# Performance work log

Hardware: AMD Instinct MI355X
Metric: run time of the kernel (lower is better)

Reference implementation:

```python
import jax, jax.numpy as jnp
import numpy as np

B, C, N = 2, 256, 8192
H = W = 64
C4 = C // 4
EPS = 1e-5


def bn(x, gamma, beta, mean, var):
    # eval-mode batchnorm over channel axis 1
    shape = (1, -1) + (1,) * (x.ndim - 2)
    inv = gamma * jax.lax.rsqrt(var + EPS)
    return x * inv.reshape(shape) + (beta - mean * inv).reshape(shape)


def conv1x1(x, w, b):
    # w: (Cout, Cin)
    return jnp.einsum('bchw,oc->bohw', x, w) + b.reshape(1, -1, 1, 1)


def conv2d(x, w, b=None, padding='VALID', groups=1, lhs_dilation=None):
    y = jax.lax.conv_general_dilated(
        x, w, window_strides=(1, 1), padding=padding,
        lhs_dilation=lhs_dilation, feature_group_count=groups,
        dimension_numbers=('NCHW', 'OIHW', 'NCHW'))
    return y if b is None else y + b.reshape(1, -1, 1, 1)


def lift_net(x, w1, b1, w2, b2, axis):
    # DAWN predictor/updater: ReflectionPad(2,1) -> conv k=4 along axis (C4->2C4)
    # -> ReLU -> 1x1 conv (2C4->C4) -> Tanh
    pad = [(0, 0)] * 4
    pad[axis] = (2, 1)
    xp = jnp.pad(x, pad, mode='reflect')
    k = w1[:, :, None, :] if axis == 3 else w1[:, :, :, None]
    h = jax.nn.relu(conv2d(xp, k, b1))
    return jnp.tanh(conv1x1(h, w2, b2))


def lifting(x, pw, axis):
    # pw = (w1, b1, w2, b2), each with leading net axis [P, U]
    w1, b1, w2, b2 = pw
    sl_e = [slice(None)] * 4; sl_e[axis] = slice(0, None, 2)
    sl_o = [slice(None)] * 4; sl_o[axis] = slice(1, None, 2)
    x_even, x_odd = x[tuple(sl_e)], x[tuple(sl_o)]
    d = x_odd - lift_net(x_even, w1[0], b1[0], w2[0], b2[0], axis)
    c = x_even + lift_net(d, w1[1], b1[1], w2[1], b2[1], axis)
    return c, d


def wavelet2d(x, w1, b1, w2, b2):
    # leading axes of weights: (scheme[horizontal, vertical], net[P, U])
    c, d = lifting(x, (w1[0], b1[0], w2[0], b2[0]), axis=3)  # split along W
    v = (w1[1], b1[1], w2[1], b2[1])                          # shared vertical weights
    LL, LH = lifting(c, v, axis=2)
    HL, HH = lifting(d, v, axis=2)
    return LL, LH, HL, HH


def convT(x, w, b):
    # torch ConvTranspose2d(k=4, stride=2, pad=1); w: (Cin, Cout, 4, 4)
    wc = jnp.flip(w, (2, 3)).transpose(1, 0, 2, 3)  # (Cout, Cin, 4, 4)
    return conv2d(x, wc, b, padding=[(2, 2), (2, 2)], lhs_dilation=(2, 2))


def _forward(tokens, flatten_mat, bn_gamma, bn_beta, bn_mean, bn_var, red_w, red_b,
             lift_w1, lift_b1, lift_w2, lift_b2,
             ff2_w1, ff2_b1, ff2_w2, ff2_b2, ct2_w, ct2_b,
             bn2_gamma, bn2_beta, bn2_mean, bn2_var,
             ff1_w1, ff1_b1, ff1_w2, ff1_b2, ct1_w, ct1_b,
             bn1_gamma, bn1_beta, bn1_mean, bn1_var,
             dw1_w, dw1_b, dw2_w, dw2_b, scale_w, inflate_idx):
    r = bn(tokens, bn_gamma, bn_beta, bn_mean, bn_var)                       # (B,C,N)
    r = jnp.einsum('bmn,bcn->bcm', flatten_mat, r).reshape(B, C, H, W)       # flatten to grid
    rr = conv1x1(r, red_w, red_b)                                            # (B,C/4,H,W)
    LL1, LH1, HL1, HH1 = wavelet2d(rr, lift_w1[0], lift_b1[0], lift_w2[0], lift_b2[0])
    LL2, LH2, HL2, HH2 = wavelet2d(LL1, lift_w1[1], lift_b1[1], lift_w2[1], lift_b2[1])
    x2 = jnp.concatenate([LL2, LH2, HL2, HH2], 1)                            # (B,C,H/4,W/4)
    y2 = conv1x1(jax.nn.gelu(conv1x1(x2, ff2_w1, ff2_b1), approximate=False), ff2_w2, ff2_b2)
    y2 = bn(convT(y2, ct2_w, ct2_b), bn2_gamma, bn2_beta, bn2_mean, bn2_var) # (B,C/2,H/2,W/2)
    x1 = jnp.concatenate([LL1, LH1, HL1, HH1, y2], 1)                        # (B,1.5C,H/2,W/2)
    y1 = conv1x1(jax.nn.gelu(conv1x1(x1, ff1_w1, ff1_b1), approximate=False), ff1_w2, ff1_b2)
    y1 = bn(convT(y1, ct1_w, ct1_b), bn1_gamma, bn1_beta, bn1_mean, bn1_var) # (B,C,H,W)
    r = r + y1
    r = conv2d(r, dw1_w, dw1_b, padding=[(1, 1), (1, 1)], groups=C)          # depthwise 3x3
    r = conv2d(jax.nn.relu(r), dw2_w, dw2_b, padding=[(1, 1), (1, 1)], groups=C)
    r = r.reshape(B, C, H * W) * scale_w.reshape(1, C, 1)                    # grouped 1x1 conv1d
    r = jnp.take_along_axis(r, inflate_idx, axis=2)                          # inflate gather
    return tokens + r


def setup_inputs() -> dict:
    key = jax.random.key(0)
    ks = iter(jax.random.split(key, 64))
    nrm = lambda shape, s=0.05: jax.random.normal(next(ks), shape, jnp.float32) * s
    uni = lambda shape: jax.random.uniform(next(ks), shape, jnp.float32, 0.5, 1.5)
    return dict(
        tokens=jax.random.normal(next(ks), (B, C, N), jnp.float32),
        flatten_mat=nrm((B, H * W, N), 0.02),
        inflate_idx=jax.random.randint(next(ks), (B, C, N), 0, H * W),
        bn_gamma=jnp.ones((C,), jnp.float32), bn_beta=jnp.zeros((C,), jnp.float32),
        bn_mean=nrm((C,), 0.1), bn_var=uni((C,)),
        red_w=nrm((C4, C)), red_b=nrm((C4,)),
        lift_w1=nrm((2, 2, 2, 2 * C4, C4, 4)), lift_b1=nrm((2, 2, 2, 2 * C4)),
        lift_w2=nrm((2, 2, 2, C4, 2 * C4)), lift_b2=nrm((2, 2, 2, C4)),
        ff2_w1=nrm((C, C)), ff2_b1=nrm((C,)), ff2_w2=nrm((C, C)), ff2_b2=nrm((C,)),
        ct2_w=nrm((C, C // 2, 4, 4)), ct2_b=nrm((C // 2,)),
        bn2_gamma=jnp.ones((C // 2,), jnp.float32), bn2_beta=jnp.zeros((C // 2,), jnp.float32),
        bn2_mean=nrm((C // 2,), 0.1), bn2_var=uni((C // 2,)),
        ff1_w1=nrm((C, C + C // 2)), ff1_b1=nrm((C,)), ff1_w2=nrm((C, C)), ff1_b2=nrm((C,)),
        ct1_w=nrm((C, C, 4, 4)), ct1_b=nrm((C,)),
        bn1_gamma=jnp.ones((C,), jnp.float32), bn1_beta=jnp.zeros((C,), jnp.float32),
        bn1_mean=nrm((C,), 0.1), bn1_var=uni((C,)),
        dw1_w=nrm((C, 1, 3, 3)), dw1_b=nrm((C,)),
        dw2_w=nrm((C, 1, 3, 3)), dw2_b=nrm((C,)),
        scale_w=nrm((C,), 0.2),
    )


def reference(tokens, flatten_mat, inflate_idx, bn_gamma, bn_beta, bn_mean, bn_var,
              red_w, red_b, lift_w1, lift_b1, lift_w2, lift_b2,
              ff2_w1, ff2_b1, ff2_w2, ff2_b2, ct2_w, ct2_b,
              bn2_gamma, bn2_beta, bn2_mean, bn2_var,
              ff1_w1, ff1_b1, ff1_w2, ff1_b2, ct1_w, ct1_b,
              bn1_gamma, bn1_beta, bn1_mean, bn1_var,
              dw1_w, dw1_b, dw2_w, dw2_b, scale_w):
    return _forward(tokens, flatten_mat, bn_gamma, bn_beta, bn_mean, bn_var, red_w, red_b,
                    lift_w1, lift_b1, lift_w2, lift_b2,
                    ff2_w1, ff2_b1, ff2_w2, ff2_b2, ct2_w, ct2_b,
                    bn2_gamma, bn2_beta, bn2_mean, bn2_var,
                    ff1_w1, ff1_b1, ff1_w2, ff1_b2, ct1_w, ct1_b,
                    bn1_gamma, bn1_beta, bn1_mean, bn1_var,
                    dw1_w, dw1_b, dw2_w, dw2_b, scale_w, inflate_idx)
```

## Files before the change

kernel.cpp:

```cpp
#include <hip/hip_runtime.h>
#include <math.h>

#define EPSV 1e-5f

typedef __attribute__((ext_vector_type(8))) short bf16x8;
typedef __attribute__((ext_vector_type(4))) float f32x4;
typedef __attribute__((ext_vector_type(8))) unsigned short u16x8;

__device__ inline unsigned short f2bf(float f) {
    unsigned u = __float_as_uint(f);
    unsigned r = (u + 0x7fffu + ((u >> 16) & 1u)) >> 16;
    return (unsigned short)r;
}

__device__ inline float bf2f(unsigned short h) {
    return __uint_as_float(((unsigned)h) << 16);
}

__device__ inline void gload_lds16(const void* g, void* l) {
    __builtin_amdgcn_global_load_lds(
        (const __attribute__((address_space(1))) void*)g,
        (__attribute__((address_space(3))) void*)l, 16, 0, 0);
}

__global__ __launch_bounds__(256) void bn_to_bf16_kernel(
    const float4* __restrict__ x, ushort4* __restrict__ y,
    const float* __restrict__ g, const float* __restrict__ be,
    const float* __restrict__ mu, const float* __restrict__ va)
{
    int i = blockIdx.x * 256 + threadIdx.x;
    int c = (i >> 11) & 255;
    float s = g[c] * rsqrtf(va[c] + EPSV);
    float t = be[c] - mu[c] * s;
    float4 v = x[i];
    ushort4 h;
    h.x = f2bf(v.x * s + t); h.y = f2bf(v.y * s + t);
    h.z = f2bf(v.z * s + t); h.w = f2bf(v.w * s + t);
    y[i] = h;
}

__global__ __launch_bounds__(256) void flatten_gemm_mfma(
    const unsigned short* __restrict__ A, const float* __restrict__ Bm,
    float* __restrict__ Pbase)
{
    __shared__ __align__(16) unsigned short AS[4][256 * 32];
    __shared__ __align__(16) unsigned short BS[4][64 * 32];
    const int NTT = 64;
    int t = threadIdx.x;
    int wid = t >> 6, lane = t & 63;
    int fid = blockIdx.z * 64 + blockIdx.x;
    int nid = (fid & 7) * 64 + (fid >> 3);
    int n0 = (nid & 63) * 64;
    int zz = nid >> 6;
    int ks = zz & 3, b = zz >> 2;
    const unsigned short* Ab = A + b * (256 * 8192);
    const float* Bb = Bm + (long)b * (4096 * 8192) + (long)n0 * 8192;
    int k0 = ks * 2048;
    int brow = t >> 3, bc8 = t & 7;
    int l15 = lane & 15, kc = lane >> 4;

    f32x4 acc[4][4] = {};

    auto issueA = [&](int tile) {
        int buf = tile & 3;
        int kb = k0 + tile * 32;
        #pragma unroll
        for (int j = 0; j < 4; ++j) {
            int d16 = (wid * 4 + j) * 64 + lane;
            int row = d16 >> 2;
            int ch = (d16 & 3) ^ ((row >> 1) & 3);
            gload_lds16(Ab + row * 8192 + kb + ch * 8, &AS[buf][(wid * 4 + j) * 512]);
        }
    };
    auto loadB = [&](int tile, float4& f0, float4& f1) {
        int kb = k0 + tile * 32;
        f0 = *(const float4*)(Bb + brow * 8192 + kb + bc8 * 4);
        f1 = *(const float4*)(Bb + (brow + 32) * 8192 + kb + bc8 * 4);
    };
    auto writeB = [&](int tile, const float4& f0, const float4& f1) {
        int buf = tile & 3;
        int ch16 = (bc8 >> 1) ^ ((brow >> 1) & 3);
        ushort4 h;
        h.x = f2bf(f0.x); h.y = f2bf(f0.y); h.z = f2bf(f0.z); h.w = f2bf(f0.w);
        *reinterpret_cast<ushort4*>(&BS[buf][brow * 32 + ch16 * 8 + (bc8 & 1) * 4]) = h;
        int rr2 = brow + 32;
        int ch16b = (bc8 >> 1) ^ ((rr2 >> 1) & 3);
        ushort4 h2;
        h2.x = f2bf(f1.x); h2.y = f2bf(f1.y); h2.z = f2bf(f1.z); h2.w = f2bf(f1.w);
        *reinterpret_cast<ushort4*>(&BS[buf][rr2 * 32 + ch16b * 8 + (bc8 & 1) * 4]) = h2;
    };
    auto mmac = [&](int tile) {
        int buf = tile & 3;
        bf16x8 af[4], bfr[4];
        #pragma unroll
        for (int mf = 0; mf < 4; ++mf) {
            int row = wid * 64 + mf * 16 + l15;
            int ch = kc ^ ((row >> 1) & 3);
            af[mf] = *reinterpret_cast<const bf16x8*>(&AS[buf][row * 32 + ch * 8]);
        }
        #pragma unroll
        for (int nf = 0; nf < 4; ++nf) {
            int row = nf * 16 + l15;
            int ch = kc ^ ((row >> 1) & 3);
            bfr[nf] = *reinterpret_cast<const bf16x8*>(&BS[buf][row * 32 + ch * 8]);
        }
        #pragma unroll
        for (int mf = 0; mf < 4; ++mf)
            #pragma unroll
            for (int nf = 0; nf < 4; ++nf)
                acc[mf][nf] = __builtin_amdgcn_mfma_f32_16x16x32_bf16(
                    af[mf], bfr[nf], acc[mf][nf], 0, 0, 0);
    };

    float4 q00, q01, q10, q11, r0, r1;
    loadB(0, q00, q01);
    loadB(1, q10, q11);
    issueA(0);
    issueA(1);

    for (int tau = 0; tau < NTT; ++tau) {
        writeB(tau, q00, q01);
        if (tau == 0)
            asm volatile("s_waitcnt vmcnt(4) lgkmcnt(0)" ::: "memory");
        else if (tau < NTT - 1)
            asm volatile("s_waitcnt vmcnt(6) lgkmcnt(0)" ::: "memory");
        else
            asm volatile("s_waitcnt vmcnt(0) lgkmcnt(0)" ::: "memory");
        __builtin_amdgcn_s_barrier();
        if (tau + 2 < NTT) {
            loadB(tau + 2, r0, r1);
            issueA(tau + 2);
        }
        mmac(tau);
        q00 = q10; q01 = q11; q10 = r0; q11 = r1;
    }

    float* P = Pbase + (long)ks * 2097152;
    float* Cb = P + (b * 256) * 4096 + n0;
    #pragma unroll
    for (int mf = 0; mf < 4; ++mf) {
        int rbase = wid * 64 + mf * 16 + (lane >> 4) * 4;
        #pragma unroll
        for (int nf = 0; nf < 4; ++nf) {
            int col = nf * 16 + (lane & 15);
            #pragma unroll
            for (int r = 0; r < 4; ++r)
                Cb[(rbase + r) * 4096 + col] = acc[mf][nf][r];
        }
    }
}

__global__ __launch_bounds__(256) void add4_t_kernel(
    const float* __restrict__ p, unsigned short* __restrict__ obf)
{
    __shared__ float tl[64][65];
    int t = threadIdx.x;
    int b = blockIdx.z;
    int c0 = blockIdx.y * 64, p0 = blockIdx.x * 64;
    #pragma unroll
    for (int u = 0; u < 16; ++u) {
        int idx = u * 256 + t;
        int cl = idx >> 6, pl = idx & 63;
        long g = (long)(b * 256 + c0 + cl) * 4096 + p0 + pl;
        tl[cl][pl] = p[g] + p[g + 2097152] + p[g + 2 * 2097152] + p[g + 3 * 2097152];
    }
    __syncthreads();
    #pragma unroll
    for (int u = 0; u < 16; ++u) {
        int idx = u * 256 + t;
        int pl = idx >> 6, cl = idx & 63;
        obf[(long)(b * 4096 + p0 + pl) * 256 + c0 + cl] = f2bf(tl[cl][pl]);
    }
}

__global__ __launch_bounds__(256) void wpack_kernel(
    const float* __restrict__ w, unsigned short* __restrict__ wp, int Cout, int Cin)
{
    int id = blockIdx.x * 256 + threadIdx.x;
    int nc8 = Cin >> 3;
    int cch = id % nc8;
    int rest = id / nc8;
    int o = rest % Cout;
    int pt = rest / Cout;
    if (pt >= 16) return;
    int par = pt >> 2, tap = pt & 3;
    int py = par >> 1, px = par & 1, u = tap >> 1, v = tap & 1;
    int tf = (3 - py - 2 * u) * 4 + (3 - px - 2 * v);
    u16x8 h;
    #pragma unroll
    for (int e = 0; e < 8; ++e)
        h[e] = f2bf(w[((cch * 8 + e) * Cout + o) * 16 + tf]);
    *reinterpret_cast<u16x8*>(&wp[((pt * Cout + o) * Cin) + cch * 8]) = h;
}

template<int NF>
__global__ __launch_bounds__(256) void conv1x1_mfma(
    const unsigned short* __restrict__ xbf, const float* __restrict__ w,
    const float* __restrict__ bias, float* __restrict__ of32,
    unsigned short* __restrict__ obf, int Cin, int Cout, int P, int act)
{
    constexpr int BP = NF * 64;
    __shared__ __align__(16) unsigned short XS[2][BP * 32];
    __shared__ __align__(16) unsigned short WS[2][64 * 32];
    int t = threadIdx.x;
    int wid = t >> 6, lane = t & 63;
    int b = blockIdx.z;
    int p0 = blockIdx.x * BP, o0 = blockIdx.y * 64;
    const unsigned short* xb = xbf + (long)b * P * Cin;
    int wm = t >> 2, wq = t & 3;
    int chunks = Cin >> 5;

    f32x4 acc[4][NF] = {};

    #pragma unroll
    for (int j = 0; j < NF; ++j) {
        int d16 = (wid * NF + j) * 64 + lane;
        int p = d16 >> 2;
        int ch = (d16 & 3) ^ ((p >> 1) & 3);
        gload_lds16(xb + (long)(p0 + p) * Cin + ch * 8, &XS[0][(wid * NF + j) * 512]);
    }
    float4 wr0 = *(const float4*)(w + (o0 + wm) * Cin + wq * 8);
    float4 wr1 = *(const float4*)(w + (o0 + wm) * Cin + wq * 8 + 4);
    __syncthreads();

    for (int cc = 0; cc < chunks; ++cc) {
        int cur = cc & 1;
        {
            int chq = wq ^ ((wm >> 1) & 3);
            u16x8 h;
            h[0] = f2bf(wr0.x); h[1] = f2bf(wr0.y); h[2] = f2bf(wr0.z); h[3] = f2bf(wr0.w);
            h[4] = f2bf(wr1.x); h[5] = f2bf(wr1.y); h[6] = f2bf(wr1.z); h[7] = f2bf(wr1.w);
            *reinterpret_cast<u16x8*>(&WS[cur][wm * 32 + chq * 8]) = h;
        }
        __syncthreads();

        if (cc < chunks - 1) {
            int kn = (cc + 1) * 32;
            #pragma unroll
            for (int j = 0; j < NF; ++j) {
                int d16 = (wid * NF + j) * 64 + lane;
                int p = d16 >> 2;
                int ch = (d16 & 3) ^ ((p >> 1) & 3);
                gload_lds16(xb + (long)(p0 + p) * Cin + kn + ch * 8,
                            &XS[cur ^ 1][(wid * NF + j) * 512]);
            }
            wr0 = *(const float4*)(w + (o0 + wm) * Cin + kn + wq * 8);
            wr1 = *(const float4*)(w + (o0 + wm) * Cin + kn + wq * 8 + 4);
        }

        int l15 = lane & 15, kc = lane >> 4;
        bf16x8 af[4], bfr[NF];
        #pragma unroll
        for (int mf = 0; mf < 4; ++mf) {
            int row = mf * 16 + l15;
            int ch = kc ^ ((row >> 1) & 3);
            af[mf] = *reinterpret_cast<const bf16x8*>(&WS[cur][row * 32 + ch * 8]);
        }
        #pragma unroll
        for (int nf = 0; nf < NF; ++nf) {
            int row = wid * (NF * 16) + nf * 16 + l15;
            int ch = kc ^ ((row >> 1) & 3);
            bfr[nf] = *reinterpret_cast<const bf16x8*>(&XS[cur][row * 32 + ch * 8]);
        }
        #pragma unroll
        for (int mf = 0; mf < 4; ++mf)
            #pragma unroll
            for (int nf = 0; nf < NF; ++nf)
                acc[mf][nf] = __builtin_amdgcn_mfma_f32_16x16x32_bf16(
                    af[mf], bfr[nf], acc[mf][nf], 0, 0, 0);
        __syncthreads();
    }

    int l15 = lane & 15, kc4 = lane >> 4;
    #pragma unroll
    for (int mf = 0; mf < 4; ++mf) {
        #pragma unroll
        for (int nf = 0; nf < NF; ++nf) {
            int p = wid * (NF * 16) + nf * 16 + l15;
            ushort4 hb;
            #pragma unroll
            for (int r = 0; r < 4; ++r) {
                int m = mf * 16 + kc4 * 4 + r;
                float v = acc[mf][nf][r] + bias[o0 + m];
                if (act == 1) v = fmaxf(v, 0.f);
                else if (act == 2) v = 0.5f * v * (1.f + erff(v * 0.70710678118f));
                if (of32) of32[((long)(b * Cout) + o0 + m) * P + p0 + p] = v;
                ((unsigned short*)&hb)[r] = f2bf(v);
            }
            if (obf)
                *reinterpret_cast<ushort4*>(
                    &obf[(long)(b * P + p0 + p) * Cout + o0 + mf * 16 + kc4 * 4]) = hb;
        }
    }
}

__global__ __launch_bounds__(256) void convt_mfma(
    const unsigned short* __restrict__ xbf, const unsigned short* __restrict__ wp,
    const float* __restrict__ bias, const float* __restrict__ g,
    const float* __restrict__ be, const float* __restrict__ mu,
    const float* __restrict__ va, const unsigned short* __restrict__ resbf,
    float* __restrict__ of32, unsigned short* __restrict__ obf,
    int Cin, int Cout, int Hin, int Win, int TR, int cshift, int OCtot, int cof)
{
    __shared__ __align__(16) unsigned short XS[165 * 32];
    __shared__ __align__(16) unsigned short WS[4 * 64 * 32];
    int t = threadIdx.x;
    int wid = t >> 6, lane = t & 63;
    int z = blockIdx.z;
    int b = z >> 2, par = z & 3;
    int py = par >> 1, px = par & 1;
    int o0 = blockIdx.y * 64;
    int i0 = blockIdx.x * TR;
    int CW = Win, CW1 = CW + 1;
    int npatch = (TR + 1) * CW1;
    int Pin = Hin * Win, Pout = 4 * Hin * Win;
    const unsigned short* xb = xbf + (long)b * Pin * Cin;
    int chunks = Cin >> 5;
    int l15 = lane & 15, kc = lane >> 4;

    f32x4 acc[4][2] = {};

    for (int cc = 0; cc < chunks; ++cc) {
        __syncthreads();
        for (int idx = t; idx < npatch * 4; idx += 256) {
            int pp = idx >> 2, ql = idx & 3;
            int qs = ql ^ ((pp >> 1) & 3);
            int a = pp / CW1, bcol = pp - a * CW1;
            int iy = i0 - (1 - py) + a;
            int ix = bcol - (1 - px);
            u16x8 v = {};
            if (iy >= 0 && iy < Hin && ix >= 0 && ix < Win)
                v = *reinterpret_cast<const u16x8*>(
                    &xb[(long)(iy * Win + ix) * Cin + cc * 32 + qs * 8]);
            *reinterpret_cast<u16x8*>(&XS[pp * 32 + ql * 8]) = v;
        }
        {
            int m = t >> 2, q = t & 3;
            int chq = q ^ ((m >> 1) & 3);
            #pragma unroll
            for (int tap = 0; tap < 4; ++tap) {
                u16x8 v = *reinterpret_cast<const u16x8*>(
                    &wp[((long)((par * 4 + tap) * Cout + o0 + m)) * Cin + cc * 32 + q * 8]);
                *reinterpret_cast<u16x8*>(&WS[tap * 2048 + m * 32 + chq * 8]) = v;
            }
        }
        __syncthreads();

        #pragma unroll
        for (int tap = 0; tap < 4; ++tap) {
            int u = tap >> 1, v = tap & 1;
            bf16x8 af[4], bfr[2];
            #pragma unroll
            for (int mf = 0; mf < 4; ++mf) {
                int row = mf * 16 + l15;
                int ch = kc ^ ((row >> 1) & 3);
                af[mf] = *reinterpret_cast<const bf16x8*>(&WS[tap * 2048 + row * 32 + ch * 8]);
            }
            #pragma unroll
            for (int nf = 0; nf < 2; ++nf) {
                int n = wid * 32 + nf * 16 + l15;
                int rn = n >> cshift, cn = n & (CW - 1);
                int pp = (rn + u) * CW1 + cn + v;
                int ch = kc ^ ((pp >> 1) & 3);
                bfr[nf] = *reinterpret_cast<const bf16x8*>(&XS[pp * 32 + ch * 8]);
            }
            #pragma unroll
            for (int mf = 0; mf < 4; ++mf)
                #pragma unroll
                for (int nf = 0; nf < 2; ++nf)
                    acc[mf][nf] = __builtin_amdgcn_mfma_f32_16x16x32_bf16(
                        af[mf], bfr[nf], acc[mf][nf], 0, 0, 0);
        }
    }

    int kc4 = lane >> 4;
    #pragma unroll
    for (int nf = 0; nf < 2; ++nf) {
        int n = wid * 32 + nf * 16 + l15;
        int rn = n >> cshift, cn = n & (CW - 1);
        int y = 2 * (i0 + rn) + py;
        int xx = 2 * cn + px;
        int pout = y * 2 * Win + xx;
        #pragma unroll
        for (int mf = 0; mf < 4; ++mf) {
            ushort4 hb;
            #pragma unroll
            for (int r = 0; r < 4; ++r) {
                int m = mf * 16 + kc4 * 4 + r;
                int o = o0 + m;
                float s = g[o] * rsqrtf(va[o] + EPSV);
                float v = (acc[mf][nf][r] + bias[o]) * s + (be[o] - mu[o] * s);
                if (resbf) v += bf2f(resbf[(long)(b * Pout + pout) * 256 + o]);
                if (of32) of32[((long)(b * Cout) + o) * Pout + pout] = v;
                ((unsigned short*)&hb)[r] = f2bf(v);
            }
            if (obf)
                *reinterpret_cast<ushort4*>(
                    &obf[(long)(b * Pout + pout) * OCtot + cof + o0 + mf * 16 + kc4 * 4]) = hb;
        }
    }
}

__global__ __launch_bounds__(1024) void lift_net_kernel(
    const float* __restrict__ xA, const float* __restrict__ xB,
    const float* __restrict__ oA, const float* __restrict__ oB,
    float* __restrict__ uA, float* __restrict__ uB,
    int x_sB, int x_sC, int x_sR, int x_sA,
    int o_sB, int o_sC, int o_sR, int o_sA,
    int u_sB, int u_sC, int u_sR, int u_sA,
    const float* __restrict__ w1, const float* __restrict__ b1,
    const float* __restrict__ w2, const float* __restrict__ b2,
    int R, int L, int lsh, float sign,
    unsigned short* __restrict__ obf, int Pb, int OCb, int cofA, int cofB)
{
    __shared__ float xsm[4864];
    __shared__ float hsm[8192];
    int t = threadIdx.x;
    int g = t & 63, ocg = t >> 6;
    int b = blockIdx.z;
    int sel = blockIdx.y;
    const float* xin = sel ? xB : xA;
    const float* oth = sel ? oB : oA;
    float* outp = sel ? uB : uA;
    int cofb = sel ? cofB : cofA;
    int rpb = 64 >> lsh;
    int row0 = blockIdx.x * rpb;
    int Lp = L + 3;
    int total = 64 * rpb * Lp;
    for (int idx = t; idx < total; idx += 1024) {
        int c = idx / (rpb * Lp);
        int rem = idx - c * rpb * Lp;
        int rr_l = rem / Lp;
        int q = rem - rr_l * Lp;
        int s = q - 2;
        s = (s < 0) ? -s : s;
        if (s >= L) s = 2 * L - 2 - s;
        xsm[idx] = xin[b * x_sB + c * x_sC + (row0 + rr_l) * x_sR + s * x_sA];
    }
    __syncthreads();

    int ocgu = __builtin_amdgcn_readfirstlane(ocg);
    int rl = g >> lsh, jl = g & (L - 1);
    const float* w1u = w1 + ocgu * 8 * 256;
    float acc1[8] = {};
    for (int c = 0; c < 64; ++c) {
        const float* xr = &xsm[(c * rpb + rl) * Lp + jl];
        float x0 = xr[0], x1 = xr[1], x2 = xr[2], x3 = xr[3];
        const float* wc = w1u + c * 4;
        #pragma unroll
        for (int k = 0; k < 8; ++k) {
            const float* wr = wc + k * 256;
            acc1[k] += wr[0] * x0 + wr[1] * x1 + wr[2] * x2 + wr[3] * x3;
        }
    }
    #pragma unroll
    for (int k = 0; k < 8; ++k) {
        int oc = ocgu * 8 + k;
        hsm[oc * 64 + g] = fmaxf(acc1[k] + b1[oc], 0.f);
    }
    __syncthreads();

    const float* w2u = w2 + ocgu * 4 * 128;
    float acc2[4] = {};
    for (int h4 = 0; h4 < 32; ++h4) {
        float hv0 = hsm[(h4 * 4 + 0) * 64 + g];
        float hv1 = hsm[(h4 * 4 + 1) * 64 + g];
        float hv2 = hsm[(h4 * 4 + 2) * 64 + g];
        float hv3 = hsm[(h4 * 4 + 3) * 64 + g];
        #pragma unroll
        for (int kk = 0; kk < 4; ++kk) {
            const float* wr = w2u + kk * 128 + h4 * 4;
            acc2[kk] += wr[0] * hv0 + wr[1] * hv1 + wr[2] * hv2 + wr[3] * hv3;
        }
    }
    int rg = row0 + rl;
    int p = rg * u_sR + jl * u_sA;
    #pragma unroll
    for (int kk = 0; kk < 4; ++kk) {
        int o = ocgu * 4 + kk;
        float v = oth[b * o_sB + o * o_sC + rg * o_sR + jl * o_sA]
                + sign * tanhf(acc2[kk] + b2[o]);
        outp[b * u_sB + o * u_sC + p] = v;
        if (obf) obf[(long)(b * Pb + p) * OCb + cofb + o] = f2bf(v);
    }
}

__global__ __launch_bounds__(256) void dw_fused_kernel(
    const float* __restrict__ r2, const float* __restrict__ w1, const float* __restrict__ b1,
    const float* __restrict__ w2, const float* __restrict__ b2v,
    const float* __restrict__ scw, const float* __restrict__ tok,
    const int* __restrict__ idx, float* __restrict__ out)
{
    __shared__ float s0[64][68];
    __shared__ float s1[64][68];
    __shared__ float s2[4096];
    int bc = blockIdx.x;
    int c = bc & 255;
    int t = threadIdx.x;
    const float* xp = r2 + (long)bc * 4096;
    for (int i = t; i < 4096; i += 256) s0[i >> 6][i & 63] = xp[i];
    float wa[9], wb[9];
    #pragma unroll
    for (int k = 0; k < 9; ++k) { wa[k] = w1[c * 9 + k]; wb[k] = w2[c * 9 + k]; }
    float ba = b1[c], bb = b2v[c], sc = scw[c];
    __syncthreads();
    for (int i = t; i < 4096; i += 256) {
        int y = i >> 6, x = i & 63;
        float a = ba;
        #pragma unroll
        for (int ky = 0; ky < 3; ++ky) {
            int yy = y + ky - 1;
            if (yy < 0 || yy > 63) continue;
            #pragma unroll
            for (int kx = 0; kx < 3; ++kx) {
                int xx = x + kx - 1;
                if (xx < 0 || xx > 63) continue;
                a += wa[ky * 3 + kx] * s0[yy][xx];
            }
        }
        s1[y][x] = fmaxf(a, 0.f);
    }
    __syncthreads();
    for (int i = t; i < 4096; i += 256) {
        int y = i >> 6, x = i & 63;
        float a = bb;
        #pragma unroll
        for (int ky = 0; ky < 3; ++ky) {
            int yy = y + ky - 1;
            if (yy < 0 || yy > 63) continue;
            #pragma unroll
            for (int kx = 0; kx < 3; ++kx) {
                int xx = x + kx - 1;
                if (xx < 0 || xx > 63) continue;
                a += wb[ky * 3 + kx] * s1[yy][xx];
            }
        }
        s2[i] = a * sc;
    }
    __syncthreads();
    long base = (long)bc << 13;
    const int4* ip = (const int4*)(idx + base);
    const float4* tp = (const float4*)(tok + base);
    float4* op = (float4*)(out + base);
    for (int i = t; i < 2048; i += 256) {
        int4 iv = ip[i];
        float4 tv = tp[i];
        float4 o;
        o.x = tv.x + s2[iv.x];
        o.y = tv.y + s2[iv.y];
        o.z = tv.z + s2[iv.z];
        o.w = tv.w + s2[iv.w];
        op[i] = o;
    }
}

extern "C" void kernel_launch(void* const* d_in, const int* in_sizes, int n_in,
                              void* d_out, int out_size, void* d_ws, size_t ws_size,
                              hipStream_t stream)
{
    const float* tokens = (const float*)d_in[0];
    const float* fm     = (const float*)d_in[1];
    const int*   infl   = (const int*)d_in[2];
    const float* bng = (const float*)d_in[3];
    const float* bnb = (const float*)d_in[4];
    const float* bnm = (const float*)d_in[5];
    const float* bnv = (const float*)d_in[6];
    const float* red_w = (const float*)d_in[7];
    const float* red_b = (const float*)d_in[8];
    const float* lw1 = (const float*)d_in[9];
    const float* lb1 = (const float*)d_in[10];
    const float* lw2 = (const float*)d_in[11];
    const float* lb2 = (const float*)d_in[12];
    const float* f2w1 = (const float*)d_in[13];
    const float* f2b1 = (const float*)d_in[14];
    const float* f2w2 = (const float*)d_in[15];
    const float* f2b2 = (const float*)d_in[16];
    const float* ct2w = (const float*)d_in[17];
    const float* ct2b = (const float*)d_in[18];
    const float* bn2g = (const float*)d_in[19];
    const float* bn2b = (const float*)d_in[20];
    const float* bn2m = (const float*)d_in[21];
    const float* bn2v = (const float*)d_in[22];
    const float* f1w1 = (const float*)d_in[23];
    const float* f1b1 = (const float*)d_in[24];
    const float* f1w2 = (const float*)d_in[25];
    const float* f1b2 = (const float*)d_in[26];
    const float* ct1w = (const float*)d_in[27];
    const float* ct1b = (const float*)d_in[28];
    const float* bn1g = (const float*)d_in[29];
    const float* bn1b = (const float*)d_in[30];
    const float* bn1m = (const float*)d_in[31];
    const float* bn1v = (const float*)d_in[32];
    const float* dw1w = (const float*)d_in[33];
    const float* dw1b = (const float*)d_in[34];
    const float* dw2w = (const float*)d_in[35];
    const float* dw2b = (const float*)d_in[36];
    const float* scw  = (const float*)d_in[37];

    float* ws = (float*)d_ws;
    unsigned short* Abf = (unsigned short*)ws;
    float* part  = ws + 2097152;
    unsigned short* rgrid_bf = (unsigned short*)(ws + 10485760);
    float* rr    = ws + 11534336;
    float* c1    = ws + 12058624;
    float* d1    = ws + 12320768;
    float* c2    = ws + 12582912;
    float* d2    = ws + 12648448;
    float* x2    = ws + 12713984;
    unsigned short* x2_bf  = (unsigned short*)(ws + 12845056);
    float* x1    = ws + 12910592;
    unsigned short* x1_bf  = (unsigned short*)(ws + 13697024);
    unsigned short* g2_bf  = (unsigned short*)(ws + 14090240);
    unsigned short* y2p_bf = (unsigned short*)(ws + 14155776);
    unsigned short* g1_bf  = (unsigned short*)(ws + 14221312);
    unsigned short* y1p_bf = (unsigned short*)(ws + 14483456);
    unsigned short* wp2    = (unsigned short*)(ws + 14745600);
    unsigned short* wp1    = (unsigned short*)(ws + 15007744);
    float* r2 = ws + 15532032;

    wpack_kernel<<<512, 256, 0, stream>>>(ct1w, wp1, 256, 256);
    wpack_kernel<<<256, 256, 0, stream>>>(ct2w, wp2, 128, 256);

    bn_to_bf16_kernel<<<4096, 256, 0, stream>>>((const float4*)tokens, (ushort4*)Abf,
                                                bng, bnb, bnm, bnv);
    flatten_gemm_mfma<<<dim3(64, 1, 8), 256, 0, stream>>>(Abf, fm, part);
    add4_t_kernel<<<dim3(64, 4, 2), 256, 0, stream>>>(part, rgrid_bf);
    conv1x1_mfma<2><<<dim3(32, 1, 2), 256, 0, stream>>>(rgrid_bf, red_w, red_b,
                                                        rr, (unsigned short*)nullptr,
                                                        256, 64, 4096, 0);

    auto lift2 = [&](const float* xA, const float* xB, const float* oA, const float* oB,
                     float* uA, float* uB,
                     int xsB, int xsC, int xsR, int xsA,
                     int osB, int osC, int osR, int osA,
                     int usB, int usC, int usR, int usA,
                     int lvl, int sch, int net, int R, int L, float sign,
                     unsigned short* obf, int Pb, int OCb, int cofA, int cofB, int nsel) {
        int widx = (lvl * 2 + sch) * 2 + net;
        int lsh = (L == 32) ? 5 : 4;
        lift_net_kernel<<<dim3(R * L / 64, nsel, 2), 1024, 0, stream>>>(
            xA, xB, oA, oB, uA, uB,
            xsB, xsC, xsR, xsA, osB, osC, osR, osA, usB, usC, usR, usA,
            lw1 + widx * 32768, lb1 + widx * 128, lw2 + widx * 8192, lb2 + widx * 64,
            R, L, lsh, sign, obf, Pb, OCb, cofA, cofB);
    };

    lift2(rr, rr, rr + 1, rr + 1, d1, d1,
          262144, 4096, 64, 2,  262144, 4096, 64, 2,  131072, 2048, 32, 1,
          0, 0, 0, 64, 32, -1.f, nullptr, 0, 0, 0, 0, 1);
    lift2(d1, d1, rr, rr, c1, c1,
          131072, 2048, 32, 1,  262144, 4096, 64, 2,  131072, 2048, 32, 1,
          0, 0, 1, 64, 32, +1.f, nullptr, 0, 0, 0, 0, 1);
    lift2(c1, d1, c1 + 32, d1 + 32, x1 + 65536, x1 + 196608,
          131072, 2048, 1, 64,  131072, 2048, 1, 64,  393216, 1024, 1, 32,
          0, 1, 0, 32, 32, -1.f, x1_bf, 1024, 384, 64, 192, 2);
    lift2(x1 + 65536, x1 + 196608, c1, d1, x1, x1 + 131072,
          393216, 1024, 1, 32,  131072, 2048, 1, 64,  393216, 1024, 1, 32,
          0, 1, 1, 32, 32, +1.f, x1_bf, 1024, 384, 0, 128, 2);
    lift2(x1, x1, x1 + 1, x1 + 1, d2, d2,
          393216, 1024, 32, 2,  393216, 1024, 32, 2,  65536, 512, 16, 1,
          1, 0, 0, 32, 16, -1.f, nullptr, 0, 0, 0, 0, 1);
    lift2(d2, d2, x1, x1, c2, c2,
          65536, 512, 16, 1,  393216, 1024, 32, 2,  65536, 512, 16, 1,
          1, 0, 1, 32, 16, +1.f, nullptr, 0, 0, 0, 0, 1);
    lift2(c2, d2, c2 + 16, d2 + 16, x2 + 16384, x2 + 49152,
          65536, 512, 1, 32,  65536, 512, 1, 32,  65536, 256, 1, 16,
          1, 1, 0, 16, 16, -1.f, x2_bf, 256, 256, 64, 192, 2);
    lift2(x2 + 16384, x2 + 49152, c2, d2, x2, x2 + 32768,
          65536, 256, 1, 16,  65536, 512, 1, 32,  65536, 256, 1, 16,
          1, 1, 1, 16, 16, +1.f, x2_bf, 256, 256, 0, 128, 2);

    conv1x1_mfma<1><<<dim3(4, 4, 2), 256, 0, stream>>>(x2_bf, f2w1, f2b1,
        (float*)nullptr, g2_bf, 256, 256, 256, 2);
    conv1x1_mfma<1><<<dim3(4, 4, 2), 256, 0, stream>>>(g2_bf, f2w2, f2b2,
        (float*)nullptr, y2p_bf, 256, 256, 256, 0);
    convt_mfma<<<dim3(2, 2, 8), 256, 0, stream>>>(y2p_bf, wp2, ct2b,
        bn2g, bn2b, bn2m, bn2v, (const unsigned short*)nullptr,
        (float*)nullptr, x1_bf, 256, 128, 16, 16, 8, 4, 384, 256);

    conv1x1_mfma<2><<<dim3(8, 4, 2), 256, 0, stream>>>(x1_bf, f1w1, f1b1,
        (float*)nullptr, g1_bf, 384, 256, 1024, 2);
    conv1x1_mfma<2><<<dim3(8, 4, 2), 256, 0, stream>>>(g1_bf, f1w2, f1b2,
        (float*)nullptr, y1p_bf, 256, 256, 1024, 0);
    convt_mfma<<<dim3(8, 4, 8), 256, 0, stream>>>(y1p_bf, wp1, ct1b,
        bn1g, bn1b, bn1m, bn1v, rgrid_bf,
        r2, (unsigned short*)nullptr, 256, 256, 32, 32, 4, 5, 0, 0);

    dw_fused_kernel<<<512, 256, 0, stream>>>(r2, dw1w, dw1b, dw2w, dw2b, scw,
                                             tokens, infl, (float*)d_out);
}
```

Measured before the change: 660.0 us.

## Fuse predict and update lifting nets into one kernel per lifting step

Merges the predictor and updater lift-net launches into a single kernel that keeps the even samples, odd samples and detail coefficients in shared memory, builds the reflection padding for d in LDS, and computes both c and d. This halves the lift launches (eight to four) and avoids writing d to global memory and reading it back. It adds LDS usage (about 88KB per block), which may limit occupancy, and serializes two nets within each block.

```diff
diff --git a/kernel.cpp b/kernel.cpp
--- a/kernel.cpp
+++ b/kernel.cpp
@@ -401,87 +401,152 @@
     }
 }
 
-__global__ __launch_bounds__(1024) void lift_net_kernel(
+__global__ __launch_bounds__(1024) void lift_pair_kernel(
     const float* __restrict__ xA, const float* __restrict__ xB,
-    const float* __restrict__ oA, const float* __restrict__ oB,
-    float* __restrict__ uA, float* __restrict__ uB,
-    int x_sB, int x_sC, int x_sR, int x_sA,
-    int o_sB, int o_sC, int o_sR, int o_sA,
+    float* __restrict__ dA, float* __restrict__ dB,
+    float* __restrict__ cA, float* __restrict__ cB,
+    int x_sB, int x_sC, int x_sR, int x_sA, int x_odd,
     int u_sB, int u_sC, int u_sR, int u_sA,
-    const float* __restrict__ w1, const float* __restrict__ b1,
-    const float* __restrict__ w2, const float* __restrict__ b2,
-    int R, int L, int lsh, float sign,
-    unsigned short* __restrict__ obf, int Pb, int OCb, int cofA, int cofB)
-{
-    __shared__ float xsm[4864];
+    const float* __restrict__ w1P, const float* __restrict__ b1P,
+    const float* __restrict__ w2P, const float* __restrict__ b2P,
+    const float* __restrict__ w1U, const float* __restrict__ b1U,
+    const float* __restrict__ w2U, const float* __restrict__ b2U,
+    int L, int lsh,
+    unsigned short* __restrict__ obf, int Pb, int OCb,
+    int cofDA, int cofCA, int cofDB, int cofCB)
+{
+    __shared__ float xsmE[4864];
+    __shared__ float xsmO[4096];
+    __shared__ float xsmD[4864];
     __shared__ float hsm[8192];
     int t = threadIdx.x;
     int g = t & 63, ocg = t >> 6;
     int b = blockIdx.z;
     int sel = blockIdx.y;
     const float* xin = sel ? xB : xA;
-    const float* oth = sel ? oB : oA;
-    float* outp = sel ? uB : uA;
-    int cofb = sel ? cofB : cofA;
+    float* dout = sel ? dB : dA;
+    float* cout_ = sel ? cB : cA;
+    int cofD = sel ? cofDB : cofDA;
+    int cofC = sel ? cofCB : cofCA;
     int rpb = 64 >> lsh;
     int row0 = blockIdx.x * rpb;
     int Lp = L + 3;
-    int total = 64 * rpb * Lp;
-    for (int idx = t; idx < total; idx += 1024) {
+    int totalE = 64 * rpb * Lp;
+    for (int idx = t; idx < totalE; idx += 1024) {
         int c = idx / (rpb * Lp);
         int rem = idx - c * rpb * Lp;
-        int rr_l = rem / Lp;
-        int q = rem - rr_l * Lp;
+        int r = rem / Lp;
+        int q = rem - r * Lp;
         int s = q - 2;
         s = (s < 0) ? -s : s;
         if (s >= L) s = 2 * L - 2 - s;
-        xsm[idx] = xin[b * x_sB + c * x_sC + (row0 + rr_l) * x_sR + s * x_sA];
+        xsmE[idx] = xin[b * x_sB + c * x_sC + (row0 + r) * x_sR + s * x_sA];
+    }
+    int totalO = 64 * rpb * L;
+    for (int idx = t; idx < totalO; idx += 1024) {
+        int c = idx / (rpb * L);
+        int rem = idx - c * rpb * L;
+        int r = rem / L;
+        int j = rem - r * L;
+        xsmO[idx] = xin[b * x_sB + c * x_sC + (row0 + r) * x_sR + j * x_sA + x_odd];
     }
     __syncthreads();
 
     int ocgu = __builtin_amdgcn_readfirstlane(ocg);
     int rl = g >> lsh, jl = g & (L - 1);
-    const float* w1u = w1 + ocgu * 8 * 256;
-    float acc1[8] = {};
-    for (int c = 0; c < 64; ++c) {
-        const float* xr = &xsm[(c * rpb + rl) * Lp + jl];
-        float x0 = xr[0], x1 = xr[1], x2 = xr[2], x3 = xr[3];
-        const float* wc = w1u + c * 4;
-        #pragma unroll
-        for (int k = 0; k < 8; ++k) {
-            const float* wr = wc + k * 256;
-            acc1[k] += wr[0] * x0 + wr[1] * x1 + wr[2] * x2 + wr[3] * x3;
-        }
-    }
-    #pragma unroll
-    for (int k = 0; k < 8; ++k) {
-        int oc = ocgu * 8 + k;
-        hsm[oc * 64 + g] = fmaxf(acc1[k] + b1[oc], 0.f);
-    }
-    __syncthreads();
-
-    const float* w2u = w2 + ocgu * 4 * 128;
-    float acc2[4] = {};
-    for (int h4 = 0; h4 < 32; ++h4) {
-        float hv0 = hsm[(h4 * 4 + 0) * 64 + g];
-        float hv1 = hsm[(h4 * 4 + 1) * 64 + g];
-        float hv2 = hsm[(h4 * 4 + 2) * 64 + g];
-        float hv3 = hsm[(h4 * 4 + 3) * 64 + g];
-        #pragma unroll
-        for (int kk = 0; kk < 4; ++kk) {
-            const float* wr = w2u + kk * 128 + h4 * 4;
-            acc2[kk] += wr[0] * hv0 + wr[1] * hv1 + wr[2] * hv2 + wr[3] * hv3;
-        }
-    }
     int rg = row0 + rl;
     int p = rg * u_sR + jl * u_sA;
-    #pragma unroll
-    for (int kk = 0; kk < 4; ++kk) {
-        int o = ocgu * 4 + kk;
-        float v = oth[b * o_sB + o * o_sC + rg * o_sR + jl * o_sA]
-                + sign * tanhf(acc2[kk] + b2[o]);
-        outp[b * u_sB + o * u_sC + p] = v;
-        if (obf) obf[(long)(b * Pb + p) * OCb + cofb + o] = f2bf(v);
+
+    {
+        const float* w1u = w1P + ocgu * 8 * 256;
+        float acc1[8] = {};
+        for (int c = 0; c < 64; ++c) {
+            const float* xr = &xsmE[(c * rpb + rl) * Lp + jl];
+            float x0 = xr[0], x1 = xr[1], x2 = xr[2], x3 = xr[3];
+            const float* wc = w1u + c * 4;
+            #pragma unroll
+            for (int k = 0; k < 8; ++k) {
+                const float* wr = wc + k * 256;
+                acc1[k] += wr[0] * x0 + wr[1] * x1 + wr[2] * x2 + wr[3] * x3;
+            }
+        }
+        #pragma unroll
+        for (int k = 0; k < 8; ++k) {
+            int oc = ocgu * 8 + k;
+            hsm[oc * 64 + g] = fmaxf(acc1[k] + b1P[oc], 0.f);
+        }
+        __syncthreads();
+        const float* w2u = w2P + ocgu * 4 * 128;
+        float acc2[4] = {};
+        for (int h4 = 0; h4 < 32; ++h4) {
+            float hv0 = hsm[(h4 * 4 + 0) * 64 + g];
+            float hv1 = hsm[(h4 * 4 + 1) * 64 + g];
+            float hv2 = hsm[(h4 * 4 + 2) * 64 + g];
+            float hv3 = hsm[(h4 * 4 + 3) * 64 + g];
+            #pragma unroll
+            for (int kk = 0; kk < 4; ++kk) {
+                const float* wr = w2u + kk * 128 + h4 * 4;
+                acc2[kk] += wr[0] * hv0 + wr[1] * hv1 + wr[2] * hv2 + wr[3] * hv3;
+            }
+        }
+        #pragma unroll
+        for (int kk = 0; kk < 4; ++kk) {
+            int o = ocgu * 4 + kk;
+            float v = xsmO[(o * rpb + rl) * L + jl] - tanhf(acc2[kk] + b2P[o]);
+            dout[b * u_sB + o * u_sC + p] = v;
+            xsmD[(o * rpb + rl) * Lp + jl + 2] = v;
+            if (obf && cofD >= 0) obf[(long)(b * Pb + p) * OCb + cofD + o] = f2bf(v);
+        }
+    }
+    __syncthreads();
+    for (int idx = t; idx < 64 * rpb; idx += 1024) {
+        float* base = &xsmD[idx * Lp];
+        base[0] = base[4];
+        base[1] = base[3];
+        base[L + 2] = base[L];
+    }
+    __syncthreads();
+
+    {
+        const float* w1u = w1U + ocgu * 8 * 256;
+        float acc1[8] = {};
+        for (int c = 0; c < 64; ++c) {
+            const float* xr = &xsmD[(c * rpb + rl) * Lp + jl];
+            float x0 = xr[0], x1 = xr[1], x2 = xr[2], x3 = xr[3];
+            const float* wc = w1u + c * 4;
+            #pragma unroll
+            for (int k = 0; k < 8; ++k) {
+                const float* wr = wc + k * 256;
+                acc1[k] += wr[0] * x0 + wr[1] * x1 + wr[2] * x2 + wr[3] * x3;
+            }
+        }
+        __syncthreads();
+        #pragma unroll
+        for (int k = 0; k < 8; ++k) {
+            int oc = ocgu * 8 + k;
+            hsm[oc * 64 + g] = fmaxf(acc1[k] + b1U[oc], 0.f);
+        }
+        __syncthreads();
+        const float* w2u = w2U + ocgu * 4 * 128;
+        float acc2[4] = {};
+        for (int h4 = 0; h4 < 32; ++h4) {
+            float hv0 = hsm[(h4 * 4 + 0) * 64 + g];
+            float hv1 = hsm[(h4 * 4 + 1) * 64 + g];
+            float hv2 = hsm[(h4 * 4 + 2) * 64 + g];
+            float hv3 = hsm[(h4 * 4 + 3) * 64 + g];
+            #pragma unroll
+            for (int kk = 0; kk < 4; ++kk) {
+                const float* wr = w2u + kk * 128 + h4 * 4;
+                acc2[kk] += wr[0] * hv0 + wr[1] * hv1 + wr[2] * hv2 + wr[3] * hv3;
+            }
+        }
+        #pragma unroll
+        for (int kk = 0; kk < 4; ++kk) {
+            int o = ocgu * 4 + kk;
+            float v = xsmE[(o * rpb + rl) * Lp + jl + 2] + tanhf(acc2[kk] + b2U[o]);
+            cout_[b * u_sB + o * u_sC + p] = v;
+            if (obf && cofC >= 0) obf[(long)(b * Pb + p) * OCb + cofC + o] = f2bf(v);
+        }
     }
 }
 
@@ -629,46 +694,36 @@
                                                         rr, (unsigned short*)nullptr,
                                                         256, 64, 4096, 0);
 
-    auto lift2 = [&](const float* xA, const float* xB, const float* oA, const float* oB,
-                     float* uA, float* uB,
-                     int xsB, int xsC, int xsR, int xsA,
-                     int osB, int osC, int osR, int osA,
+    auto lpair = [&](const float* xA, const float* xB,
+                     float* dA, float* dB, float* cA, float* cB,
+                     int xsB, int xsC, int xsR, int xsA, int xodd,
                      int usB, int usC, int usR, int usA,
-                     int lvl, int sch, int net, int R, int L, float sign,
-                     unsigned short* obf, int Pb, int OCb, int cofA, int cofB, int nsel) {
-        int widx = (lvl * 2 + sch) * 2 + net;
+                     int lvl, int sch, int L, int nsel,
+                     unsigned short* obf, int Pb, int OCb,
+                     int cofDA, int cofCA, int cofDB, int cofCB, int nblk) {
+        int wP = (lvl * 2 + sch) * 2;
+        int wU = wP + 1;
         int lsh = (L == 32) ? 5 : 4;
-        lift_net_kernel<<<dim3(R * L / 64, nsel, 2), 1024, 0, stream>>>(
-            xA, xB, oA, oB, uA, uB,
-            xsB, xsC, xsR, xsA, osB, osC, osR, osA, usB, usC, usR, usA,
-            lw1 + widx * 32768, lb1 + widx * 128, lw2 + widx * 8192, lb2 + widx * 64,
-            R, L, lsh, sign, obf, Pb, OCb, cofA, cofB);
+        lift_pair_kernel<<<dim3(nblk, nsel, 2), 1024, 0, stream>>>(
+            xA, xB, dA, dB, cA, cB,
+            xsB, xsC, xsR, xsA, xodd, usB, usC, usR, usA,
+            lw1 + wP * 32768, lb1 + wP * 128, lw2 + wP * 8192, lb2 + wP * 64,
+            lw1 + wU * 32768, lb1 + wU * 128, lw2 + wU * 8192, lb2 + wU * 64,
+            L, lsh, obf, Pb, OCb, cofDA, cofCA, cofDB, cofCB);
     };
 
-    lift2(rr, rr, rr + 1, rr + 1, d1, d1,
-          262144, 4096, 64, 2,  262144, 4096, 64, 2,  131072, 2048, 32, 1,
-          0, 0, 0, 64, 32, -1.f, nullptr, 0, 0, 0, 0, 1);
-    lift2(d1, d1, rr, rr, c1, c1,
-          131072, 2048, 32, 1,  262144, 4096, 64, 2,  131072, 2048, 32, 1,
-          0, 0, 1, 64, 32, +1.f, nullptr, 0, 0, 0, 0, 1);
-    lift2(c1, d1, c1 + 32, d1 + 32, x1 + 65536, x1 + 196608,
-          131072, 2048, 1, 64,  131072, 2048, 1, 64,  393216, 1024, 1, 32,
-          0, 1, 0, 32, 32, -1.f, x1_bf, 1024, 384, 64, 192, 2);
-    lift2(x1 + 65536, x1 + 196608, c1, d1, x1, x1 + 131072,
-          393216, 1024, 1, 32,  131072, 2048, 1, 64,  393216, 1024, 1, 32,
-          0, 1, 1, 32, 32, +1.f, x1_bf, 1024, 384, 0, 128, 2);
-    lift2(x1, x1, x1 + 1, x1 + 1, d2, d2,
-          393216, 1024, 32, 2,  393216, 1024, 32, 2,  65536, 512, 16, 1,
-          1, 0, 0, 32, 16, -1.f, nullptr, 0, 0, 0, 0, 1);
-    lift2(d2, d2, x1, x1, c2, c2,
-          65536, 512, 16, 1,  393216, 1024, 32, 2,  65536, 512, 16, 1,
-          1, 0, 1, 32, 16, +1.f, nullptr, 0, 0, 0, 0, 1);
-    lift2(c2, d2, c2 + 16, d2 + 16, x2 + 16384, x2 + 49152,
-          65536, 512, 1, 32,  65536, 512, 1, 32,  65536, 256, 1, 16,
-          1, 1, 0, 16, 16, -1.f, x2_bf, 256, 256, 64, 192, 2);
-    lift2(x2 + 16384, x2 + 49152, c2, d2, x2, x2 + 32768,
-          65536, 256, 1, 16,  65536, 512, 1, 32,  65536, 256, 1, 16,
-          1, 1, 1, 16, 16, +1.f, x2_bf, 256, 256, 0, 128, 2);
+    lpair(rr, rr, d1, d1, c1, c1,
+          262144, 4096, 64, 2, 1,  131072, 2048, 32, 1,
+          0, 0, 32, 1, nullptr, 0, 0, -1, -1, -1, -1, 32);
+    lpair(c1, d1, x1 + 65536, x1 + 196608, x1, x1 + 131072,
+          131072, 2048, 1, 64, 32,  393216, 1024, 1, 32,
+          0, 1, 32, 2, x1_bf, 1024, 384, 64, 0, 192, 128, 16);
+    lpair(x1, x1, d2, d2, c2, c2,
+          393216, 1024, 32, 2, 1,  65536, 512, 16, 1,
+          1, 0, 16, 1, nullptr, 0, 0, -1, -1, -1, -1, 8);
+    lpair(c2, d2, x2 + 16384, x2 + 49152, x2, x2 + 32768,
+          65536, 512, 1, 32, 16,  65536, 256, 1, 16,
+          1, 1, 16, 2, x2_bf, 256, 256, 64, 0, 192, 128, 4);
 
     conv1x1_mfma<1><<<dim3(4, 4, 2), 256, 0, stream>>>(x2_bf, f2w1, f2b1,
         (float*)nullptr, g2_bf, 256, 256, 256, 2);
```

Result: slower. 676.5 us (+2.5%).
